# Performance work log

Measured on AMD Instinct MI355X. Metric: run time of the kernel, lower is better.

Reference implementation:

```python
import jax, jax.numpy as jnp
import numpy as np
import math

D_MODEL = 256
N_LEVELS = 4
N_HEADS = 8
N_POINTS = 4
N_FRAME = 4
SHAPES = [(80, 80), (40, 40), (20, 20), (10, 10)]  # sum H*W = 8500
NB = 2
T1 = 4
T2 = 4
LEN_Q = 8500


def _grid_init_bias():
    # replicate torch _reset_parameters grid bias for sampling_offsets
    thetas = np.arange(N_HEADS, dtype=np.float32) * (2.0 * math.pi / N_HEADS)
    grid = np.stack([np.cos(thetas), np.sin(thetas)], -1)
    grid = grid / np.abs(grid).max(-1, keepdims=True)
    grid = np.tile(grid[:, None, None, :], (1, N_LEVELS, N_POINTS, 1))
    grid = grid * (np.arange(N_POINTS, dtype=np.float32) + 1.0)[None, None, :, None]
    return jnp.asarray(grid.reshape(-1), jnp.float32)


def setup_inputs() -> dict:
    key = jax.random.key(0)
    ks = jax.random.split(key, 8)
    Len_in = sum(h * w for h, w in SHAPES)
    query = jax.random.normal(ks[0], (NB, T1, LEN_Q, D_MODEL), jnp.float32)
    reference_points = jax.random.uniform(ks[1], (NB, T1, LEN_Q, N_LEVELS, 2), jnp.float32)
    input_flatten = jax.random.normal(ks[2], (NB, T2, Len_in, D_MODEL), jnp.float32)
    input_spatial_shapes = jnp.array(SHAPES, jnp.int32)
    starts = np.cumsum([0] + [h * w for h, w in SHAPES])[:-1]
    input_level_start_index = jnp.asarray(starts, jnp.int32)
    s = 0.01
    W_off = jax.random.normal(ks[3], (D_MODEL, N_HEADS * N_LEVELS * N_POINTS * 2), jnp.float32) * s
    b_off = _grid_init_bias()
    W_att = jax.random.normal(ks[4], (D_MODEL, N_HEADS * N_LEVELS * N_POINTS), jnp.float32) * s
    b_att = jnp.zeros((N_HEADS * N_LEVELS * N_POINTS,), jnp.float32)
    xav = 1.0 / math.sqrt(D_MODEL)
    W_val = jax.random.normal(ks[5], (D_MODEL, D_MODEL), jnp.float32) * xav
    b_val = jnp.zeros((D_MODEL,), jnp.float32)
    W_out = jax.random.normal(ks[6], (D_MODEL, D_MODEL), jnp.float32) * xav
    b_out = jnp.zeros((D_MODEL,), jnp.float32)
    return dict(query=query, reference_points=reference_points, input_flatten=input_flatten,
                input_spatial_shapes=input_spatial_shapes, input_level_start_index=input_level_start_index,
                W_off=W_off, b_off=b_off, W_att=W_att, b_att=b_att,
                W_val=W_val, b_val=b_val, W_out=W_out, b_out=b_out)


def _bilinear(v_flat, H, W, gx, gy):
    # v_flat: (B, d, H*W); gx,gy: (B, S) in [-1,1]; zeros padding, align_corners=False
    x = (gx + 1.0) * (W * 0.5) - 0.5
    y = (gy + 1.0) * (H * 0.5) - 0.5
    x0 = jnp.floor(x); y0 = jnp.floor(y)
    x1 = x0 + 1.0; y1 = y0 + 1.0
    wx1 = x - x0; wx0 = 1.0 - wx1
    wy1 = y - y0; wy0 = 1.0 - wy1

    def gather(xi, yi):
        valid = ((xi >= 0) & (xi < W) & (yi >= 0) & (yi < H)).astype(v_flat.dtype)
        xc = jnp.clip(xi, 0, W - 1).astype(jnp.int32)
        yc = jnp.clip(yi, 0, H - 1).astype(jnp.int32)
        idx = yc * W + xc  # (B, S)
        g = jnp.take_along_axis(v_flat, idx[:, None, :], axis=2)  # (B, d, S)
        return g * valid[:, None, :]

    return (gather(x0, y0) * (wx0 * wy0)[:, None, :]
            + gather(x1, y0) * (wx1 * wy0)[:, None, :]
            + gather(x0, y1) * (wx0 * wy1)[:, None, :]
            + gather(x1, y1) * (wx1 * wy1)[:, None, :])


def _core(value_t, locs, att, shapes):
    # value_t: (n, Len_in, M, d); locs: (n, Lq, M, L, P, 2); att: (n, Lq, M, L, P)
    n, Len_in, M, d = value_t.shape
    Lq, P = locs.shape[1], locs.shape[4]
    start = 0
    out = 0.0
    for l, (H, W) in enumerate(shapes):
        hw = H * W
        v = value_t[:, start:start + hw]  # (n, hw, M, d)
        start += hw
        v = v.transpose(0, 2, 3, 1).reshape(n * M, d, hw)
        g = locs[:, :, :, l] * 2.0 - 1.0  # (n, Lq, M, P, 2)
        g = g.transpose(0, 2, 1, 3, 4).reshape(n * M, Lq * P, 2)
        samp = _bilinear(v, H, W, g[..., 0], g[..., 1])  # (n*M, d, Lq*P)
        a = att[:, :, :, l].transpose(0, 2, 1, 3).reshape(n * M, 1, Lq * P)
        out = out + (samp * a).reshape(n, M, d, Lq, P).sum(-1)
    return out.transpose(0, 3, 1, 2).reshape(n, Lq, M * d)  # (n, Lq, C)


def reference(query, reference_points, input_flatten, input_spatial_shapes, input_level_start_index,
              W_off, b_off, W_att, b_att, W_val, b_val, W_out, b_out):
    shapes = [(int(h), int(w)) for h, w in np.asarray(input_spatial_shapes)]
    n, t1n, Lq, C = query.shape
    M, L, P = N_HEADS, N_LEVELS, N_POINTS
    d = C // M
    value = input_flatten @ W_val + b_val  # (n, T2, Len_in, C)
    value = value.reshape(n, value.shape[1], -1, M, d)
    normalizer = jnp.array([[w, h] for h, w in shapes], jnp.float32)  # (L, 2) = (W_l, H_l)
    outs = []
    for t1 in range(t1n):
        t2s = [t for t in (t1 - 1, t1, t1 + 1) if 0 <= t < N_FRAME]
        K = len(t2s)
        q = query[:, t1]  # (n, Lq, C)
        # all frames share ONE attention_weights Linear -> identical logits per t2
        logits = (q @ W_att + b_att).reshape(n, Lq, M, L, P)
        stacked = jnp.broadcast_to(logits[..., None], (n, Lq, M, L, P, K))
        att = jax.nn.softmax(stacked.reshape(n, Lq, M, L * P * K), axis=-1)
        att = att.reshape(n, Lq, M, L, P, K)
        # all frames share ONE sampling_offsets Linear -> identical locations per t2
        off = (q @ W_off + b_off).reshape(n, Lq, M, L, P, 2)
        off = off / normalizer[None, None, None, :, None, :]
        locs = reference_points[:, t1][:, :, None, :, None, :] + off  # (n,Lq,M,L,P,2)
        out_t1 = 0.0
        for k, t2 in enumerate(t2s):
            out_t1 = out_t1 + _core(value[:, t2], locs, att[..., k], shapes)
        outs.append(out_t1)
    out = jnp.stack(outs, axis=1)  # (n, T1, Lq, C)
    return out @ W_out + b_out
```

## Files before the change

kernel.cpp:

```cpp
#include <hip/hip_runtime.h>

#define LQ 8500

typedef _Float16 half8 __attribute__((ext_vector_type(8)));
typedef float f32x4 __attribute__((ext_vector_type(4)));

__device__ __forceinline__ unsigned short f2h(float f) {
    return __builtin_bit_cast(unsigned short, (_Float16)f);
}
__device__ __forceinline__ float hlo(unsigned w) {
    return (float)__builtin_bit_cast(_Float16, (unsigned short)(w & 0xffffu));
}
__device__ __forceinline__ float hhi(unsigned w) {
    return (float)__builtin_bit_cast(_Float16, (unsigned short)(w >> 16));
}
__device__ __forceinline__ unsigned pk2(float a, float b) {
    return (unsigned)f2h(a) | ((unsigned)f2h(b) << 16);
}

__global__ __launch_bounds__(256) void prep_weights(const float* __restrict__ Woff,
                                                    const float* __restrict__ boff,
                                                    const float* __restrict__ Watt,
                                                    const float* __restrict__ batt,
                                                    const float* __restrict__ Wval,
                                                    const float* __restrict__ Wout,
                                                    unsigned short* __restrict__ Wct,
                                                    unsigned short* __restrict__ Wvt,
                                                    unsigned short* __restrict__ Wot,
                                                    float* __restrict__ bcat) {
    int idx = blockIdx.x * 256 + threadIdx.x;
    if (idx < 98304) {
        int j = idx >> 8, k = idx & 255;
        float v = (j < 256) ? Woff[k * 256 + j] : Watt[k * 128 + (j - 256)];
        Wct[idx] = f2h(v);
    } else if (idx < 98304 + 65536) {
        int t = idx - 98304;
        int n = t >> 8, k = t & 255;
        Wvt[t] = f2h(Wval[k * 256 + n]);
    } else if (idx < 98304 + 131072) {
        int t = idx - 98304 - 65536;
        int n = t >> 8, k = t & 255;
        Wot[t] = f2h(Wout[k * 256 + n]);
    } else if (idx < 98304 + 131072 + 384) {
        int j = idx - 98304 - 131072;
        bcat[j] = (j < 256) ? boff[j] : batt[j - 256];
    }
}

__global__ __launch_bounds__(256) void conv_f32_f16(const float4* __restrict__ in,
                                                    uint4* __restrict__ out, int n8) {
    int i = blockIdx.x * 256 + threadIdx.x;
    if (i >= n8) return;
    float4 a = in[2 * i], b = in[2 * i + 1];
    uint4 o;
    o.x = pk2(a.x, a.y); o.y = pk2(a.z, a.w);
    o.z = pk2(b.x, b.y); o.w = pk2(b.z, b.w);
    out[i] = o;
}

__global__ __launch_bounds__(256) void sum_frames(const float4* __restrict__ inp,
                                                  uint4* __restrict__ Xs) {
    int g = blockIdx.y;
    int t1 = g & 3, n = g >> 2;
    int f = blockIdx.x * 256 + threadIdx.x;
    if (f >= LQ * 32) return;
    int t2a = t1 == 0 ? 0 : t1 - 1;
    int t2b = t1 == 3 ? 3 : t1 + 1;
    float4 s0 = {0, 0, 0, 0}, s1 = {0, 0, 0, 0};
    for (int t2 = t2a; t2 <= t2b; ++t2) {
        const float4* p = inp + (size_t)(n * 4 + t2) * (LQ * 64) + (size_t)f * 2;
        float4 a = p[0], b = p[1];
        s0.x += a.x; s0.y += a.y; s0.z += a.z; s0.w += a.w;
        s1.x += b.x; s1.y += b.y; s1.z += b.z; s1.w += b.w;
    }
    uint4 o;
    o.x = pk2(s0.x, s0.y); o.y = pk2(s0.z, s0.w);
    o.z = pk2(s1.x, s1.y); o.w = pk2(s1.z, s1.w);
    Xs[(size_t)g * (LQ * 32) + f] = o;
}

template <int OUTMODE>
__global__ __launch_bounds__(256) void gemm_f16(const unsigned short* __restrict__ A,
                                                const unsigned short* __restrict__ Bt,
                                                const float* __restrict__ bias,
                                                void* __restrict__ Cout, int M) {
    __shared__ char lds[16384];
    const int tid = threadIdx.x;
    const int r0 = blockIdx.x * 128, c0 = blockIdx.y * 128;
    const int wid = tid >> 6, lane = tid & 63;
    const int wr = (wid >> 1) * 64, wc = (wid & 1) * 64;

    f32x4 acc[4][4] = {};

    for (int k0 = 0; k0 < 256; k0 += 32) {
#pragma unroll
        for (int cc = 0; cc < 2; ++cc) {
            int ch = cc * 256 + tid;
            int row = ch >> 2, seg = ch & 3;
            int byte = (row << 6) + (seg << 4);
            int swz = byte ^ ((row & 7) << 4);
            uint4 va = {0, 0, 0, 0};
            int ar = r0 + row;
            if (ar < M)
                va = *reinterpret_cast<const uint4*>(A + (size_t)ar * 256 + k0 + seg * 8);
            *reinterpret_cast<uint4*>(lds + swz) = va;
            uint4 vb = *reinterpret_cast<const uint4*>(Bt + (size_t)(c0 + row) * 256 + k0 + seg * 8);
            *reinterpret_cast<uint4*>(lds + 8192 + swz) = vb;
        }
        __syncthreads();
        half8 af[4], bf[4];
#pragma unroll
        for (int i = 0; i < 4; ++i) {
            int rowA = wr + i * 16 + (lane & 15);
            int byteA = (rowA << 6) + ((lane >> 4) << 4);
            af[i] = *reinterpret_cast<const half8*>(lds + (byteA ^ ((rowA & 7) << 4)));
            int rowB = wc + i * 16 + (lane & 15);
            int byteB = (rowB << 6) + ((lane >> 4) << 4);
            bf[i] = *reinterpret_cast<const half8*>(lds + 8192 + (byteB ^ ((rowB & 7) << 4)));
        }
#pragma unroll
        for (int i = 0; i < 4; ++i)
#pragma unroll
            for (int j = 0; j < 4; ++j)
                acc[i][j] = __builtin_amdgcn_mfma_f32_16x16x32_f16(af[i], bf[j], acc[i][j], 0, 0, 0);
        __syncthreads();
    }

#pragma unroll
    for (int j = 0; j < 4; ++j) {
        int col = c0 + wc + j * 16 + (lane & 15);
        float bv = bias[col];
#pragma unroll
        for (int i = 0; i < 4; ++i) {
#pragma unroll
            for (int r = 0; r < 4; ++r) {
                int row = r0 + wr + i * 16 + (lane >> 4) * 4 + r;
                if (row >= M) continue;
                float v = acc[i][j][r];
                if (OUTMODE == 1) {
                    int g = row / LQ;
                    int pos = row - g * LQ;
                    int t1 = g & 3;
                    float sc = (t1 == 0 || t1 == 3) ? 2.f : 3.f;
                    v += bv * sc;
                    int m = col >> 5, c = col & 31;
                    ((unsigned short*)Cout)[((size_t)(g * 8 + m) * LQ + pos) * 32 + c] = f2h(v);
                } else if (OUTMODE == 2) {
                    ((unsigned short*)Cout)[(size_t)row * 384 + col] = f2h(v + bv);
                } else {
                    ((float*)Cout)[(size_t)row * 256 + col] = v + bv;
                }
            }
        }
    }
}

__global__ __launch_bounds__(256) void sample_kernel(const unsigned short* __restrict__ P,
                                                     const float* __restrict__ refp,
                                                     const unsigned short* __restrict__ Vs,
                                                     unsigned short* __restrict__ O16) {
    int tid = threadIdx.x, bid = blockIdx.x;
    int g = bid & 7;
    int q0 = (bid >> 3) * 16;
    int ql = tid >> 4, m = (tid >> 1) & 7, h = tid & 1;
    int q = q0 + ql;
    if (q >= LQ) return;

    const size_t qrow = (size_t)g * LQ + q;

    unsigned ow[16];
    {
        const uint4* po = reinterpret_cast<const uint4*>(P + qrow * 384 + m * 32);
        uint4 a = po[0], b = po[1], c = po[2], d = po[3];
        ow[0] = a.x; ow[1] = a.y; ow[2] = a.z; ow[3] = a.w;
        ow[4] = b.x; ow[5] = b.y; ow[6] = b.z; ow[7] = b.w;
        ow[8] = c.x; ow[9] = c.y; ow[10] = c.z; ow[11] = c.w;
        ow[12] = d.x; ow[13] = d.y; ow[14] = d.z; ow[15] = d.w;
    }
    float wgt[16];
    {
        const uint4* pa = reinterpret_cast<const uint4*>(P + qrow * 384 + 256 + m * 16);
        uint4 a = pa[0], b = pa[1];
        unsigned aw[8] = {a.x, a.y, a.z, a.w, b.x, b.y, b.z, b.w};
#pragma unroll
        for (int j = 0; j < 8; ++j) {
            wgt[j * 2 + 0] = hlo(aw[j]);
            wgt[j * 2 + 1] = hhi(aw[j]);
        }
        float mx = -1e30f;
#pragma unroll
        for (int j = 0; j < 16; ++j) mx = fmaxf(mx, wgt[j]);
        float s = 0.f;
#pragma unroll
        for (int j = 0; j < 16; ++j) { wgt[j] = __expf(wgt[j] - mx); s += wgt[j]; }
        int t1 = g & 3;
        float Kc = (t1 == 0 || t1 == 3) ? 2.f : 3.f;
        float inv = 1.f / (s * Kc);
#pragma unroll
        for (int j = 0; j < 16; ++j) wgt[j] *= inv;
    }

    float rx[4], ry[4];
    {
        const float4* rp = reinterpret_cast<const float4*>(refp + qrow * 8);
        float4 r0 = rp[0], r1 = rp[1];
        rx[0] = r0.x; ry[0] = r0.y; rx[1] = r0.z; ry[1] = r0.w;
        rx[2] = r1.x; ry[2] = r1.y; rx[3] = r1.z; ry[3] = r1.w;
    }

    float acc[16];
#pragma unroll
    for (int d = 0; d < 16; ++d) acc[d] = 0.f;

    const unsigned short* vplane = Vs + (size_t)(g * 8 + m) * (LQ * 32) + h * 16;

#pragma unroll
    for (int p = 0; p < 16; ++p) {
        const int l = p >> 2;
        const int Wl = 80 >> l;
        const int start = (l == 0) ? 0 : (l == 1) ? 6400 : (l == 2) ? 8000 : 8400;
        const float Wlf = (float)Wl;

        float x = fmaf(rx[l], Wlf, hlo(ow[p])) - 0.5f;
        float y = fmaf(ry[l], Wlf, hhi(ow[p])) - 0.5f;
        float w = wgt[p];

        float xf = floorf(x), yf = floorf(y);
        int x0 = (int)xf, y0 = (int)yf;
        float wx1 = x - xf, wy1 = y - yf;

        int xb = min(max(x0, 0), Wl - 2);
        float wl = (x0 == xb) ? 1.f - wx1 : ((x0 + 1 == xb) ? wx1 : 0.f);
        float wr = (x0 == xb) ? wx1 : ((x0 - 1 == xb) ? 1.f - wx1 : 0.f);

        int yc[2];
        float cw[2];
        yc[0] = min(max(y0, 0), Wl - 1);
        cw[0] = (y0 >= 0 && y0 < Wl) ? (1.f - wy1) * w : 0.f;
        int y1i = y0 + 1;
        yc[1] = min(max(y1i, 0), Wl - 1);
        cw[1] = (y1i >= 0 && y1i < Wl) ? wy1 * w : 0.f;

#pragma unroll
        for (int ryi = 0; ryi < 2; ++ryi) {
            float cl = cw[ryi] * wl, cr = cw[ryi] * wr;
            const uint4* vp = reinterpret_cast<const uint4*>(
                vplane + (size_t)(start + yc[ryi] * Wl + xb) * 32);
            uint4 La = vp[0], Lb = vp[1];
            uint4 Ra = vp[4], Rb = vp[5];
            acc[0]  += cl * hlo(La.x) + cr * hlo(Ra.x);
            acc[1]  += cl * hhi(La.x) + cr * hhi(Ra.x);
            acc[2]  += cl * hlo(La.y) + cr * hlo(Ra.y);
            acc[3]  += cl * hhi(La.y) + cr * hhi(Ra.y);
            acc[4]  += cl * hlo(La.z) + cr * hlo(Ra.z);
            acc[5]  += cl * hhi(La.z) + cr * hhi(Ra.z);
            acc[6]  += cl * hlo(La.w) + cr * hlo(Ra.w);
            acc[7]  += cl * hhi(La.w) + cr * hhi(Ra.w);
            acc[8]  += cl * hlo(Lb.x) + cr * hlo(Rb.x);
            acc[9]  += cl * hhi(Lb.x) + cr * hhi(Rb.x);
            acc[10] += cl * hlo(Lb.y) + cr * hlo(Rb.y);
            acc[11] += cl * hhi(Lb.y) + cr * hhi(Rb.y);
            acc[12] += cl * hlo(Lb.z) + cr * hlo(Rb.z);
            acc[13] += cl * hhi(Lb.z) + cr * hhi(Rb.z);
            acc[14] += cl * hlo(Lb.w) + cr * hlo(Rb.w);
            acc[15] += cl * hhi(Lb.w) + cr * hhi(Rb.w);
        }
    }

    unsigned short* op = O16 + qrow * 256 + m * 32 + h * 16;
    uint4 o0, o1;
    o0.x = pk2(acc[0], acc[1]);   o0.y = pk2(acc[2], acc[3]);
    o0.z = pk2(acc[4], acc[5]);   o0.w = pk2(acc[6], acc[7]);
    o1.x = pk2(acc[8], acc[9]);   o1.y = pk2(acc[10], acc[11]);
    o1.z = pk2(acc[12], acc[13]); o1.w = pk2(acc[14], acc[15]);
    reinterpret_cast<uint4*>(op)[0] = o0;
    reinterpret_cast<uint4*>(op)[1] = o1;
}

extern "C" void kernel_launch(void* const* d_in, const int* in_sizes, int n_in,
                              void* d_out, int out_size, void* d_ws, size_t ws_size,
                              hipStream_t stream) {
    const float* query = (const float*)d_in[0];
    const float* refp  = (const float*)d_in[1];
    const float* inp   = (const float*)d_in[2];
    const float* Woff = (const float*)d_in[5];
    const float* boff = (const float*)d_in[6];
    const float* Watt = (const float*)d_in[7];
    const float* batt = (const float*)d_in[8];
    const float* Wval = (const float*)d_in[9];
    const float* bval = (const float*)d_in[10];
    const float* Wout = (const float*)d_in[11];
    const float* bout = (const float*)d_in[12];
    float* out = (float*)d_out;

    char* base = (char*)d_ws;
    unsigned short* Xs16 = (unsigned short*)base;
    unsigned short* Vs   = (unsigned short*)(base + 34816000);
    unsigned short* P    = (unsigned short*)(base + 69632000);
    unsigned short* Wct  = (unsigned short*)(base + 121856000);
    unsigned short* Wvt  = (unsigned short*)(base + 122052608);
    unsigned short* Wot  = (unsigned short*)(base + 122183680);
    float* bcat          = (float*)(base + 122314752);
    unsigned short* O16  = Xs16;
    unsigned short* q16  = (unsigned short*)d_out;

    prep_weights<<<dim3(898), 256, 0, stream>>>(Woff, boff, Watt, batt, Wval, Wout,
                                                Wct, Wvt, Wot, bcat);

    conv_f32_f16<<<dim3(8500), 256, 0, stream>>>((const float4*)query, (uint4*)q16,
                                                 17408000 / 8);

    sum_frames<<<dim3((LQ * 32 + 255) / 256, 8), 256, 0, stream>>>(
        (const float4*)inp, (uint4*)Xs16);

    gemm_f16<1><<<dim3((8 * LQ + 127) / 128, 2), 256, 0, stream>>>(
        Xs16, Wvt, bval, Vs, 8 * LQ);

    gemm_f16<2><<<dim3((8 * LQ + 127) / 128, 3), 256, 0, stream>>>(
        q16, Wct, bcat, P, 8 * LQ);

    sample_kernel<<<dim3(((LQ + 15) / 16) * 8), 256, 0, stream>>>(P, refp, Vs, O16);

    gemm_f16<0><<<dim3((8 * LQ + 127) / 128, 2), 256, 0, stream>>>(
        O16, Wot, bout, out, 8 * LQ);
}
```

Baseline: 337.9 us.

## Fuse f32-to-f16 conversion and frame summation into GEMM loads with double-buffered LDS

Removes the standalone query conversion and frame-summing kernels. The value and projection GEMMs now read fp32 inputs directly, summing neighbouring frames and converting to half inside the tile load. The GEMM main loop gains register-staged prefetch into a double-buffered LDS tile so global loads overlap the MFMA work. The sampling kernel issues all four corner loads per point up front and only partially unrolls the point loop. In exchange, the GEMMs re-read fp32 data, up to three frames per tile for the value GEMM, since column blocks each redo the conversion, and LDS use doubles.

```diff
diff --git a/kernel.cpp b/kernel.cpp
--- a/kernel.cpp
+++ b/kernel.cpp
@@ -47,82 +47,99 @@
     }
 }
 
-__global__ __launch_bounds__(256) void conv_f32_f16(const float4* __restrict__ in,
-                                                    uint4* __restrict__ out, int n8) {
-    int i = blockIdx.x * 256 + threadIdx.x;
-    if (i >= n8) return;
-    float4 a = in[2 * i], b = in[2 * i + 1];
-    uint4 o;
-    o.x = pk2(a.x, a.y); o.y = pk2(a.z, a.w);
-    o.z = pk2(b.x, b.y); o.w = pk2(b.z, b.w);
-    out[i] = o;
-}
-
-__global__ __launch_bounds__(256) void sum_frames(const float4* __restrict__ inp,
-                                                  uint4* __restrict__ Xs) {
-    int g = blockIdx.y;
-    int t1 = g & 3, n = g >> 2;
-    int f = blockIdx.x * 256 + threadIdx.x;
-    if (f >= LQ * 32) return;
-    int t2a = t1 == 0 ? 0 : t1 - 1;
-    int t2b = t1 == 3 ? 3 : t1 + 1;
-    float4 s0 = {0, 0, 0, 0}, s1 = {0, 0, 0, 0};
-    for (int t2 = t2a; t2 <= t2b; ++t2) {
-        const float4* p = inp + (size_t)(n * 4 + t2) * (LQ * 64) + (size_t)f * 2;
-        float4 a = p[0], b = p[1];
-        s0.x += a.x; s0.y += a.y; s0.z += a.z; s0.w += a.w;
-        s1.x += b.x; s1.y += b.y; s1.z += b.z; s1.w += b.w;
-    }
-    uint4 o;
-    o.x = pk2(s0.x, s0.y); o.y = pk2(s0.z, s0.w);
-    o.z = pk2(s1.x, s1.y); o.w = pk2(s1.z, s1.w);
-    Xs[(size_t)g * (LQ * 32) + f] = o;
-}
-
-template <int OUTMODE>
-__global__ __launch_bounds__(256) void gemm_f16(const unsigned short* __restrict__ A,
+template <int OUTMODE, int ASRC>
+__global__ __launch_bounds__(256) void gemm_f16(const void* __restrict__ Avoid,
                                                 const unsigned short* __restrict__ Bt,
                                                 const float* __restrict__ bias,
                                                 void* __restrict__ Cout, int M) {
-    __shared__ char lds[16384];
+    __shared__ char lds[32768];
     const int tid = threadIdx.x;
     const int r0 = blockIdx.x * 128, c0 = blockIdx.y * 128;
     const int wid = tid >> 6, lane = tid & 63;
     const int wr = (wid >> 1) * 64, wc = (wid & 1) * 64;
 
     f32x4 acc[4][4] = {};
-
-    for (int k0 = 0; k0 < 256; k0 += 32) {
-#pragma unroll
-        for (int cc = 0; cc < 2; ++cc) {
-            int ch = cc * 256 + tid;
-            int row = ch >> 2, seg = ch & 3;
-            int byte = (row << 6) + (seg << 4);
-            int swz = byte ^ ((row & 7) << 4);
-            uint4 va = {0, 0, 0, 0};
-            int ar = r0 + row;
-            if (ar < M)
-                va = *reinterpret_cast<const uint4*>(A + (size_t)ar * 256 + k0 + seg * 8);
-            *reinterpret_cast<uint4*>(lds + swz) = va;
-            uint4 vb = *reinterpret_cast<const uint4*>(Bt + (size_t)(c0 + row) * 256 + k0 + seg * 8);
-            *reinterpret_cast<uint4*>(lds + 8192 + swz) = vb;
-        }
-        __syncthreads();
+    uint4 ra[2], rb[2];
+
+#define LOADT(k0)                                                                      \
+    {                                                                                  \
+        _Pragma("unroll")                                                              \
+        for (int cc = 0; cc < 2; ++cc) {                                               \
+            int ch = cc * 256 + tid;                                                   \
+            int row = ch >> 2, seg = ch & 3;                                           \
+            uint4 va = {0, 0, 0, 0};                                                   \
+            int ar = r0 + row;                                                         \
+            if (ar < M) {                                                              \
+                if (ASRC == 0) {                                                       \
+                    va = *reinterpret_cast<const uint4*>(                              \
+                        (const unsigned short*)Avoid + (size_t)ar * 256 + (k0) + seg * 8); \
+                } else if (ASRC == 1) {                                                \
+                    const float4* ap = reinterpret_cast<const float4*>(                \
+                        (const float*)Avoid + (size_t)ar * 256 + (k0) + seg * 8);      \
+                    float4 a = ap[0], b = ap[1];                                       \
+                    va.x = pk2(a.x, a.y); va.y = pk2(a.z, a.w);                        \
+                    va.z = pk2(b.x, b.y); va.w = pk2(b.z, b.w);                        \
+                } else {                                                               \
+                    int g = ar / LQ;                                                   \
+                    int pos = ar - g * LQ;                                             \
+                    int t1 = g & 3, n = g >> 2;                                        \
+                    int t2a = t1 == 0 ? 0 : t1 - 1;                                    \
+                    int t2b = t1 == 3 ? 3 : t1 + 1;                                    \
+                    float4 s0 = {0, 0, 0, 0}, s1 = {0, 0, 0, 0};                       \
+                    for (int t2 = t2a; t2 <= t2b; ++t2) {                              \
+                        const float4* p = reinterpret_cast<const float4*>(             \
+                            (const float*)Avoid +                                      \
+                            ((size_t)(n * 4 + t2) * LQ + pos) * 256 + (k0) + seg * 8); \
+                        float4 a = p[0], b = p[1];                                     \
+                        s0.x += a.x; s0.y += a.y; s0.z += a.z; s0.w += a.w;            \
+                        s1.x += b.x; s1.y += b.y; s1.z += b.z; s1.w += b.w;            \
+                    }                                                                  \
+                    va.x = pk2(s0.x, s0.y); va.y = pk2(s0.z, s0.w);                    \
+                    va.z = pk2(s1.x, s1.y); va.w = pk2(s1.z, s1.w);                    \
+                }                                                                      \
+            }                                                                          \
+            ra[cc] = va;                                                               \
+            rb[cc] = *reinterpret_cast<const uint4*>(Bt + (size_t)(c0 + row) * 256 +   \
+                                                     (k0) + seg * 8);                  \
+        }                                                                              \
+    }
+
+#define STORET(b)                                                                      \
+    {                                                                                  \
+        _Pragma("unroll")                                                              \
+        for (int cc = 0; cc < 2; ++cc) {                                               \
+            int ch = cc * 256 + tid;                                                   \
+            int row = ch >> 2, seg = ch & 3;                                           \
+            int byte = (row << 6) + (seg << 4);                                        \
+            int swz = byte ^ ((row & 7) << 4);                                         \
+            *reinterpret_cast<uint4*>(lds + (b) * 16384 + swz) = ra[cc];               \
+            *reinterpret_cast<uint4*>(lds + (b) * 16384 + 8192 + swz) = rb[cc];        \
+        }                                                                              \
+    }
+
+    LOADT(0);
+    STORET(0);
+    __syncthreads();
+
+    for (int t = 0; t < 8; ++t) {
+        if (t < 7) LOADT((t + 1) * 32);
+        char* base = lds + (t & 1) * 16384;
         half8 af[4], bf[4];
 #pragma unroll
         for (int i = 0; i < 4; ++i) {
             int rowA = wr + i * 16 + (lane & 15);
             int byteA = (rowA << 6) + ((lane >> 4) << 4);
-            af[i] = *reinterpret_cast<const half8*>(lds + (byteA ^ ((rowA & 7) << 4)));
+            af[i] = *reinterpret_cast<const half8*>(base + (byteA ^ ((rowA & 7) << 4)));
             int rowB = wc + i * 16 + (lane & 15);
             int byteB = (rowB << 6) + ((lane >> 4) << 4);
-            bf[i] = *reinterpret_cast<const half8*>(lds + 8192 + (byteB ^ ((rowB & 7) << 4)));
+            bf[i] = *reinterpret_cast<const half8*>(base + 8192 + (byteB ^ ((rowB & 7) << 4)));
         }
 #pragma unroll
         for (int i = 0; i < 4; ++i)
 #pragma unroll
             for (int j = 0; j < 4; ++j)
                 acc[i][j] = __builtin_amdgcn_mfma_f32_16x16x32_f16(af[i], bf[j], acc[i][j], 0, 0, 0);
+        if (t < 7) STORET((t + 1) & 1);
         __syncthreads();
     }
 
@@ -153,6 +170,8 @@
             }
         }
     }
+#undef LOADT
+#undef STORET
 }
 
 __global__ __launch_bounds__(256) void sample_kernel(const unsigned short* __restrict__ P,
@@ -214,7 +233,7 @@
 
     const unsigned short* vplane = Vs + (size_t)(g * 8 + m) * (LQ * 32) + h * 16;
 
-#pragma unroll
+#pragma unroll 4
     for (int p = 0; p < 16; ++p) {
         const int l = p >> 2;
         const int Wl = 80 >> l;
@@ -233,38 +252,38 @@
         float wl = (x0 == xb) ? 1.f - wx1 : ((x0 + 1 == xb) ? wx1 : 0.f);
         float wr = (x0 == xb) ? wx1 : ((x0 - 1 == xb) ? 1.f - wx1 : 0.f);
 
-        int yc[2];
-        float cw[2];
-        yc[0] = min(max(y0, 0), Wl - 1);
-        cw[0] = (y0 >= 0 && y0 < Wl) ? (1.f - wy1) * w : 0.f;
+        int yc0 = min(max(y0, 0), Wl - 1);
+        float cw0 = (y0 >= 0 && y0 < Wl) ? (1.f - wy1) * w : 0.f;
         int y1i = y0 + 1;
-        yc[1] = min(max(y1i, 0), Wl - 1);
-        cw[1] = (y1i >= 0 && y1i < Wl) ? wy1 * w : 0.f;
-
-#pragma unroll
-        for (int ryi = 0; ryi < 2; ++ryi) {
-            float cl = cw[ryi] * wl, cr = cw[ryi] * wr;
-            const uint4* vp = reinterpret_cast<const uint4*>(
-                vplane + (size_t)(start + yc[ryi] * Wl + xb) * 32);
-            uint4 La = vp[0], Lb = vp[1];
-            uint4 Ra = vp[4], Rb = vp[5];
-            acc[0]  += cl * hlo(La.x) + cr * hlo(Ra.x);
-            acc[1]  += cl * hhi(La.x) + cr * hhi(Ra.x);
-            acc[2]  += cl * hlo(La.y) + cr * hlo(Ra.y);
-            acc[3]  += cl * hhi(La.y) + cr * hhi(Ra.y);
-            acc[4]  += cl * hlo(La.z) + cr * hlo(Ra.z);
-            acc[5]  += cl * hhi(La.z) + cr * hhi(Ra.z);
-            acc[6]  += cl * hlo(La.w) + cr * hlo(Ra.w);
-            acc[7]  += cl * hhi(La.w) + cr * hhi(Ra.w);
-            acc[8]  += cl * hlo(Lb.x) + cr * hlo(Rb.x);
-            acc[9]  += cl * hhi(Lb.x) + cr * hhi(Rb.x);
-            acc[10] += cl * hlo(Lb.y) + cr * hlo(Rb.y);
-            acc[11] += cl * hhi(Lb.y) + cr * hhi(Rb.y);
-            acc[12] += cl * hlo(Lb.z) + cr * hlo(Rb.z);
-            acc[13] += cl * hhi(Lb.z) + cr * hhi(Rb.z);
-            acc[14] += cl * hlo(Lb.w) + cr * hlo(Rb.w);
-            acc[15] += cl * hhi(Lb.w) + cr * hhi(Rb.w);
-        }
+        int yc1 = min(max(y1i, 0), Wl - 1);
+        float cw1 = (y1i >= 0 && y1i < Wl) ? wy1 * w : 0.f;
+
+        const uint4* p0 = reinterpret_cast<const uint4*>(
+            vplane + (size_t)(start + yc0 * Wl + xb) * 32);
+        const uint4* p1 = reinterpret_cast<const uint4*>(
+            vplane + (size_t)(start + yc1 * Wl + xb) * 32);
+        uint4 L0a = p0[0], L0b = p0[1], R0a = p0[4], R0b = p0[5];
+        uint4 L1a = p1[0], L1b = p1[1], R1a = p1[4], R1b = p1[5];
+
+        float c0l = cw0 * wl, c0r = cw0 * wr;
+        float c1l = cw1 * wl, c1r = cw1 * wr;
+
+        acc[0]  += c0l * hlo(L0a.x) + c0r * hlo(R0a.x) + c1l * hlo(L1a.x) + c1r * hlo(R1a.x);
+        acc[1]  += c0l * hhi(L0a.x) + c0r * hhi(R0a.x) + c1l * hhi(L1a.x) + c1r * hhi(R1a.x);
+        acc[2]  += c0l * hlo(L0a.y) + c0r * hlo(R0a.y) + c1l * hlo(L1a.y) + c1r * hlo(R1a.y);
+        acc[3]  += c0l * hhi(L0a.y) + c0r * hhi(R0a.y) + c1l * hhi(L1a.y) + c1r * hhi(R1a.y);
+        acc[4]  += c0l * hlo(L0a.z) + c0r * hlo(R0a.z) + c1l * hlo(L1a.z) + c1r * hlo(R1a.z);
+        acc[5]  += c0l * hhi(L0a.z) + c0r * hhi(R0a.z) + c1l * hhi(L1a.z) + c1r * hhi(R1a.z);
+        acc[6]  += c0l * hlo(L0a.w) + c0r * hlo(R0a.w) + c1l * hlo(L1a.w) + c1r * hlo(R1a.w);
+        acc[7]  += c0l * hhi(L0a.w) + c0r * hhi(R0a.w) + c1l * hhi(L1a.w) + c1r * hhi(R1a.w);
+        acc[8]  += c0l * hlo(L0b.x) + c0r * hlo(R0b.x) + c1l * hlo(L1b.x) + c1r * hlo(R1b.x);
+        acc[9]  += c0l * hhi(L0b.x) + c0r * hhi(R0b.x) + c1l * hhi(L1b.x) + c1r * hhi(R1b.x);
+        acc[10] += c0l * hlo(L0b.y) + c0r * hlo(R0b.y) + c1l * hlo(L1b.y) + c1r * hlo(R1b.y);
+        acc[11] += c0l * hhi(L0b.y) + c0r * hhi(R0b.y) + c1l * hhi(L1b.y) + c1r * hhi(R1b.y);
+        acc[12] += c0l * hlo(L0b.z) + c0r * hlo(R0b.z) + c1l * hlo(L1b.z) + c1r * hlo(R1b.z);
+        acc[13] += c0l * hhi(L0b.z) + c0r * hhi(R0b.z) + c1l * hhi(L1b.z) + c1r * hhi(R1b.z);
+        acc[14] += c0l * hlo(L0b.w) + c0r * hlo(R0b.w) + c1l * hlo(L1b.w) + c1r * hlo(R1b.w);
+        acc[15] += c0l * hhi(L0b.w) + c0r * hhi(R0b.w) + c1l * hhi(L1b.w) + c1r * hhi(R1b.w);
     }
 
     unsigned short* op = O16 + qrow * 256 + m * 32 + h * 16;
@@ -294,33 +313,25 @@
     float* out = (float*)d_out;
 
     char* base = (char*)d_ws;
-    unsigned short* Xs16 = (unsigned short*)base;
-    unsigned short* Vs   = (unsigned short*)(base + 34816000);
-    unsigned short* P    = (unsigned short*)(base + 69632000);
+    unsigned short* Vs   = (unsigned short*)base;
+    unsigned short* P    = (unsigned short*)(base + 34816000);
+    unsigned short* O16  = (unsigned short*)(base + 87040000);
     unsigned short* Wct  = (unsigned short*)(base + 121856000);
     unsigned short* Wvt  = (unsigned short*)(base + 122052608);
     unsigned short* Wot  = (unsigned short*)(base + 122183680);
     float* bcat          = (float*)(base + 122314752);
-    unsigned short* O16  = Xs16;
-    unsigned short* q16  = (unsigned short*)d_out;
 
     prep_weights<<<dim3(898), 256, 0, stream>>>(Woff, boff, Watt, batt, Wval, Wout,
                                                 Wct, Wvt, Wot, bcat);
 
-    conv_f32_f16<<<dim3(8500), 256, 0, stream>>>((const float4*)query, (uint4*)q16,
-                                                 17408000 / 8);
-
-    sum_frames<<<dim3((LQ * 32 + 255) / 256, 8), 256, 0, stream>>>(
-        (const float4*)inp, (uint4*)Xs16);
-
-    gemm_f16<1><<<dim3((8 * LQ + 127) / 128, 2), 256, 0, stream>>>(
-        Xs16, Wvt, bval, Vs, 8 * LQ);
-
-    gemm_f16<2><<<dim3((8 * LQ + 127) / 128, 3), 256, 0, stream>>>(
-        q16, Wct, bcat, P, 8 * LQ);
+    gemm_f16<1, 2><<<dim3((8 * LQ + 127) / 128, 2), 256, 0, stream>>>(
+        inp, Wvt, bval, Vs, 8 * LQ);
+
+    gemm_f16<2, 1><<<dim3((8 * LQ + 127) / 128, 3), 256, 0, stream>>>(
+        query, Wct, bcat, P, 8 * LQ);
 
     sample_kernel<<<dim3(((LQ + 15) / 16) * 8), 256, 0, stream>>>(P, refp, Vs, O16);
 
-    gemm_f16<0><<<dim3((8 * LQ + 127) / 128, 2), 256, 0, stream>>>(
+    gemm_f16<0, 0><<<dim3((8 * LQ + 127) / 128, 2), 256, 0, stream>>>(
         O16, Wot, bout, out, 8 * LQ);
 }
```

Result: slower. 360.8 us (+6.8%).
